# Kernel tuning notes

Hardware: AMD Instinct MI355X
Metric: run time of the kernel (lower is better)

## Reference

```python
import jax, jax.numpy as jnp
import numpy as np

N_NODES = 100000
N_EDGES = 1200000
IN_DIM, HID, OUT = 128, 64, 64


def setup_inputs() -> dict:
    key = jax.random.key(0)
    ks = jax.random.split(key, 16)
    s = 0.05
    return {
        "x": jax.random.normal(ks[0], (N_NODES, IN_DIM), jnp.float32),
        "fc_w": jax.random.normal(ks[1], (IN_DIM, HID), jnp.float32) * s,
        "fc_b": jnp.zeros((HID,), jnp.float32),
        "conv1_w": jax.random.normal(ks[2], (IN_DIM, HID), jnp.float32) * s,
        "conv1_b": jnp.zeros((HID,), jnp.float32),
        "fc1_w": jax.random.normal(ks[3], (2 * HID, OUT), jnp.float32) * s,
        "fc1_b": jnp.zeros((OUT,), jnp.float32),
        "conv2_w": jax.random.normal(ks[4], (2 * HID, OUT), jnp.float32) * s,
        "conv2_b": jnp.zeros((OUT,), jnp.float32),
        "fc2_w": jax.random.normal(ks[5], (OUT, 1), jnp.float32) * s,
        "fc2_b": jnp.zeros((1,), jnp.float32),
        "conv3_w": jax.random.normal(ks[6], (OUT, 1), jnp.float32) * s,
        "conv3_b": jnp.zeros((1,), jnp.float32),
        "edge_index": jax.random.randint(ks[7], (2, N_EDGES), 0, N_NODES, jnp.int64 if jax.config.jax_enable_x64 else jnp.int32),
    }


def gcn_conv(h_in, w, b, row, col, norm, n_nodes):
    # PyG GCNConv (no self loops): scatter_add(norm * (XW)[row]) at col, + bias
    h = h_in @ w                                  # [N, F_out]
    msg = h[row] * norm[:, None]                  # [E, F_out]
    out = jax.ops.segment_sum(msg, col, num_segments=n_nodes)
    return out + b


def reference(x, fc_w, fc_b, conv1_w, conv1_b, fc1_w, fc1_b, conv2_w, conv2_b,
              fc2_w, fc2_b, conv3_w, conv3_b, edge_index):
    n = x.shape[0]
    row, col = edge_index[0], edge_index[1]
    # symmetric normalization: deg over destination nodes (unit edge weights)
    deg = jax.ops.segment_sum(jnp.ones(row.shape[0], x.dtype), col, num_segments=n)
    dinv = jnp.where(deg > 0, jax.lax.rsqrt(jnp.maximum(deg, 1.0)), 0.0)
    norm = dinv[row] * dinv[col]                  # [E]

    x1 = jax.nn.relu(x @ fc_w + fc_b)             # MLP branch [N, HID]
    x2 = jax.nn.relu(gcn_conv(x, conv1_w, conv1_b, row, col, norm, n))
    x3 = jnp.concatenate([x1, x2], axis=1)        # [N, 2*HID]
    x5 = jax.nn.relu(x3 @ fc1_w + fc1_b)
    x6 = jax.nn.relu(gcn_conv(x3, conv2_w, conv2_b, row, col, norm, n))
    x7 = x5 + x6                                  # residual combine [N, OUT]
    x9 = x7 @ fc2_w + fc2_b
    x10 = gcn_conv(x7, conv3_w, conv3_b, row, col, norm, n)
    return x9 + x10                               # [N, 1]
```

## Files before the change

### kernel.cpp

```cpp
#include <hip/hip_runtime.h>

#define IN_DIM 128
#define HID 64
#define RB_SHIFT 10
#define RB 1024
#define NBMAX 128
#define MAXBIN 16384
#define PCH 2048

typedef short bf16x8 __attribute__((ext_vector_type(8)));
typedef float f32x4  __attribute__((ext_vector_type(4)));

__device__ __forceinline__ float relu(float v) { return v > 0.f ? v : 0.f; }

__device__ __forceinline__ unsigned short f2bf(float f) {
    unsigned u = __float_as_uint(f);
    u += 0x7FFFu + ((u >> 16) & 1u);
    return (unsigned short)(u >> 16);
}
__device__ __forceinline__ float bflo(unsigned u) { return __uint_as_float(u << 16); }
__device__ __forceinline__ float bfhi(unsigned u) { return __uint_as_float(u & 0xFFFF0000u); }

__global__ __launch_bounds__(256) void k_wprep(const float* __restrict__ W1a,
                                               const float* __restrict__ W2a,
                                               const float* __restrict__ W1b,
                                               const float* __restrict__ W2b,
                                               unsigned short* __restrict__ Wt,
                                               int* __restrict__ binCursor, int NR) {
    if (blockIdx.x == 0 && threadIdx.x < NR) binCursor[threadIdx.x] = threadIdx.x * MAXBIN;
    const int t = blockIdx.x * 256 + threadIdx.x;
    if (t >= 2 * 4 * 8 * 64) return;
    const int lane = t & 63;
    const int c = (t >> 6) & 7;
    const int kc = (t >> 9) & 3;
    const int layer = t >> 11;
    const int col = c * 16 + (lane & 15);
    const int k0 = kc * 32 + (lane >> 4) * 8;
    const float* W1 = layer ? W1b : W1a;
    const float* W2 = layer ? W2b : W2a;
    const float* src = (col < 64) ? (W1 + col) : (W2 + (col - 64));
    unsigned short v[8];
#pragma unroll
    for (int j = 0; j < 8; j++) v[j] = f2bf(src[(size_t)(k0 + j) * 64]);
    *(ushort4*)(Wt + (size_t)t * 8) = make_ushort4(v[0], v[1], v[2], v[3]);
    *(ushort4*)(Wt + (size_t)t * 8 + 4) = make_ushort4(v[4], v[5], v[6], v[7]);
}

__global__ __launch_bounds__(256) void k_part(const int* __restrict__ row,
                                              const int* __restrict__ col,
                                              int* __restrict__ binCursor,
                                              int2* __restrict__ part, int E) {
    __shared__ int lcur[NBMAX], gbase[NBMAX];
    const int tid = threadIdx.x;
    const int e0 = blockIdx.x * PCH;
    const int cnt = min(PCH, E - e0);
    if (tid < NBMAX) lcur[tid] = 0;
    __syncthreads();
    int rr[8], cc[8], pp[8];
    if (cnt == PCH) {
#pragma unroll
        for (int h = 0; h < 2; h++) {
            const int4 c4 = *(const int4*)(col + e0 + h * 1024 + tid * 4);
            const int4 r4 = *(const int4*)(row + e0 + h * 1024 + tid * 4);
            cc[h * 4 + 0] = c4.x; cc[h * 4 + 1] = c4.y;
            cc[h * 4 + 2] = c4.z; cc[h * 4 + 3] = c4.w;
            rr[h * 4 + 0] = r4.x; rr[h * 4 + 1] = r4.y;
            rr[h * 4 + 2] = r4.z; rr[h * 4 + 3] = r4.w;
        }
    } else {
#pragma unroll
        for (int j = 0; j < 8; j++) {
            const int e = e0 + j * 256 + tid;
            if (e < e0 + cnt) { rr[j] = row[e]; cc[j] = col[e]; }
            else cc[j] = -1;
        }
    }
#pragma unroll
    for (int j = 0; j < 8; j++)
        if (cc[j] >= 0) pp[j] = atomicAdd(&lcur[cc[j] >> RB_SHIFT], 1);
    __syncthreads();
    if (tid < NBMAX && lcur[tid] > 0)
        gbase[tid] = atomicAdd(&binCursor[tid], lcur[tid]);
    __syncthreads();
#pragma unroll
    for (int j = 0; j < 8; j++)
        if (cc[j] >= 0)
            part[gbase[cc[j] >> RB_SHIFT] + pp[j]] = make_int2(rr[j], cc[j]);
}

__global__ __launch_bounds__(256) void k_csrA(const int* __restrict__ binCursor,
                                              const int2* __restrict__ part,
                                              int* __restrict__ degi,
                                              float* __restrict__ dinv,
                                              int* __restrict__ start, int N) {
    __shared__ int cnt[RB];
    __shared__ int psum[256];
    const int b = blockIdx.x;
    const int lo = b << RB_SHIFT;
    const int tid = threadIdx.x;
    for (int i = tid; i < RB; i += 256) cnt[i] = 0;
    __syncthreads();
    const int base = b * MAXBIN;
    const int tot = binCursor[b] - base;
    for (int i = tid; i < tot; i += 256)
        atomicAdd(&cnt[part[base + i].y - lo], 1);
    __syncthreads();
    const int i0 = tid * 4;
    const int c0 = cnt[i0], c1 = cnt[i0 + 1], c2 = cnt[i0 + 2], c3 = cnt[i0 + 3];
    const int s = c0 + c1 + c2 + c3;
    psum[tid] = s;
    __syncthreads();
    for (int off = 1; off < 256; off <<= 1) {
        int t = (tid >= off) ? psum[tid - off] : 0;
        __syncthreads();
        psum[tid] += t;
        __syncthreads();
    }
    const int e = psum[tid] - s;
    const int offs[4] = {e, e + c0, e + c0 + c1, e + c0 + c1 + c2};
    const int cs[4] = {c0, c1, c2, c3};
#pragma unroll
    for (int j = 0; j < 4; j++) {
        const int n = lo + i0 + j;
        if (n < N) {
            degi[n] = cs[j];
            start[n] = base + offs[j];
            dinv[n] = cs[j] > 0 ? rsqrtf((float)cs[j]) : 0.f;
        }
    }
}

__global__ __launch_bounds__(256) void k_csrB(const int* __restrict__ binCursor,
                                              const int2* __restrict__ part,
                                              const int* __restrict__ start,
                                              const float* __restrict__ dinv,
                                              int2* __restrict__ rw, int N) {
    __shared__ int curs[RB];
    __shared__ float dv[RB];
    const int b = blockIdx.x;
    const int lo = b << RB_SHIFT;
    const int tid = threadIdx.x;
    for (int i = tid; i < RB; i += 256) {
        const int n = lo + i;
        curs[i] = (n < N) ? start[n] : 0;
        dv[i] = (n < N) ? dinv[n] : 0.f;
    }
    __syncthreads();
    const int base = b * MAXBIN;
    const int tot = binCursor[b] - base;
    for (int i = tid; i < tot; i += 256) {
        const int2 v = part[base + i];
        const int li = v.y - lo;
        const int pos = atomicAdd(&curs[li], 1);
        rw[pos] = make_int2(v.x, __float_as_int(dinv[v.x] * dv[li]));
    }
}

template <int LAYER>
__global__ __launch_bounds__(256) void k_gemm(const float* __restrict__ XF,
                                              const unsigned short* __restrict__ X1B,
                                              const unsigned short* __restrict__ X2B,
                                              const unsigned short* __restrict__ Wt,
                                              const float* __restrict__ B1,
                                              float* __restrict__ O1f,
                                              unsigned short* __restrict__ O1b,
                                              unsigned short* __restrict__ O2,
                                              int N) {
    const int tid = threadIdx.x;
    const int wave = tid >> 6;
    const int lane = tid & 63;
    const int quad = lane >> 4;
    const int lm = lane & 15;
    const int n0 = blockIdx.x * 64 + wave * 16;
    if (n0 >= N) return;
    const int nrow = min(n0 + lm, N - 1);

    f32x4 acc[8];
#pragma unroll
    for (int c = 0; c < 8; c++) acc[c] = (f32x4){0.f, 0.f, 0.f, 0.f};

#pragma unroll
    for (int kc = 0; kc < 4; kc++) {
        const int k0 = kc * 32 + quad * 8;
        bf16x8 a;
        if (LAYER == 1) {
            const float* s = XF + (size_t)nrow * IN_DIM + k0;
            const float4 q0 = *(const float4*)s;
            const float4 q1 = *(const float4*)(s + 4);
            a[0] = (short)f2bf(q0.x); a[1] = (short)f2bf(q0.y);
            a[2] = (short)f2bf(q0.z); a[3] = (short)f2bf(q0.w);
            a[4] = (short)f2bf(q1.x); a[5] = (short)f2bf(q1.y);
            a[6] = (short)f2bf(q1.z); a[7] = (short)f2bf(q1.w);
        } else {
            const unsigned short* s = (kc < 2) ? (X1B + (size_t)nrow * 64 + k0)
                                               : (X2B + (size_t)nrow * 64 + (k0 - 64));
            a = *(const bf16x8*)s;
        }
#pragma unroll
        for (int c = 0; c < 8; c++) {
            const bf16x8 b = *(const bf16x8*)(Wt + (size_t)((kc * 8 + c) * 64 + lane) * 8);
            acc[c] = __builtin_amdgcn_mfma_f32_16x16x32_bf16(a, b, acc[c], 0, 0, 0);
        }
    }

    const int nb = n0 + quad * 4;
#pragma unroll
    for (int c = 0; c < 4; c++) {
        const int col = c * 16 + lm;
        const float b = B1[col];
#pragma unroll
        for (int r = 0; r < 4; r++) {
            const int n = nb + r;
            if (n < N) {
                const float v = relu(acc[c][r] + b);
                if (LAYER == 1) O1b[(size_t)n * 64 + col] = f2bf(v);
                else            O1f[(size_t)n * 64 + col] = v;
            }
        }
    }
#pragma unroll
    for (int c = 4; c < 8; c++) {
        const int col = (c - 4) * 16 + lm;
#pragma unroll
        for (int r = 0; r < 4; r++) {
            const int n = nb + r;
            if (n < N) O2[(size_t)n * 64 + col] = f2bf(acc[c][r]);
        }
    }
}

template <int MODE>
__global__ __launch_bounds__(256) void k_gather(const int* __restrict__ start,
                                                const int* __restrict__ degi,
                                                const int2* __restrict__ rw,
                                                const unsigned short* __restrict__ H,
                                                const float* __restrict__ CB,
                                                unsigned short* __restrict__ OXB,
                                                const float* __restrict__ X5,
                                                const float* __restrict__ FC2W,
                                                const float* __restrict__ FC2B,
                                                const float* __restrict__ C3W,
                                                const float* __restrict__ C3B,
                                                float* __restrict__ H3,
                                                float* __restrict__ OUT, int N) {
    const int l = threadIdx.x & 15;
    const int d = blockIdx.x * 16 + (threadIdx.x >> 4);
    if (d >= N) return;
    int s = start[d];
    const int e2 = s + degi[d];
    float a0 = 0.f, a1 = 0.f, a2 = 0.f, a3 = 0.f;
    for (; s + 3 < e2; s += 4) {
        const int2 ea = rw[s], eb = rw[s + 1], ec = rw[s + 2], ed = rw[s + 3];
        const uint2 ua = *(const uint2*)(H + (size_t)ea.x * 64 + l * 4);
        const uint2 ub = *(const uint2*)(H + (size_t)eb.x * 64 + l * 4);
        const uint2 uc = *(const uint2*)(H + (size_t)ec.x * 64 + l * 4);
        const uint2 ud = *(const uint2*)(H + (size_t)ed.x * 64 + l * 4);
        const float wa = __int_as_float(ea.y), wb = __int_as_float(eb.y);
        const float wc = __int_as_float(ec.y), wd = __int_as_float(ed.y);
        a0 += wa * bflo(ua.x); a1 += wa * bfhi(ua.x);
        a2 += wa * bflo(ua.y); a3 += wa * bfhi(ua.y);
        a0 += wb * bflo(ub.x); a1 += wb * bfhi(ub.x);
        a2 += wb * bflo(ub.y); a3 += wb * bfhi(ub.y);
        a0 += wc * bflo(uc.x); a1 += wc * bfhi(uc.x);
        a2 += wc * bflo(uc.y); a3 += wc * bfhi(uc.y);
        a0 += wd * bflo(ud.x); a1 += wd * bfhi(ud.x);
        a2 += wd * bflo(ud.y); a3 += wd * bfhi(ud.y);
    }
    for (; s < e2; ++s) {
        const int2 ea = rw[s];
        const uint2 ua = *(const uint2*)(H + (size_t)ea.x * 64 + l * 4);
        const float wa = __int_as_float(ea.y);
        a0 += wa * bflo(ua.x); a1 += wa * bfhi(ua.x);
        a2 += wa * bflo(ua.y); a3 += wa * bfhi(ua.y);
    }
    const float4 cb = *(const float4*)(CB + l * 4);
    if (MODE == 1) {
        ushort4 o;
        o.x = f2bf(relu(a0 + cb.x)); o.y = f2bf(relu(a1 + cb.y));
        o.z = f2bf(relu(a2 + cb.z)); o.w = f2bf(relu(a3 + cb.w));
        *(ushort4*)(OXB + (size_t)d * 64 + l * 4) = o;
    } else {
        const float4 x5v = *(const float4*)(X5 + (size_t)d * 64 + l * 4);
        const float v0 = x5v.x + relu(a0 + cb.x);
        const float v1 = x5v.y + relu(a1 + cb.y);
        const float v2 = x5v.z + relu(a2 + cb.z);
        const float v3 = x5v.w + relu(a3 + cb.w);
        const float4 w9 = *(const float4*)(FC2W + l * 4);
        const float4 wX = *(const float4*)(C3W + l * 4);
        float p9 = v0 * w9.x + v1 * w9.y + v2 * w9.z + v3 * w9.w;
        float p10 = v0 * wX.x + v1 * wX.y + v2 * wX.z + v3 * wX.w;
#pragma unroll
        for (int m = 1; m < 16; m <<= 1) {
            p9 += __shfl_xor(p9, m, 64);
            p10 += __shfl_xor(p10, m, 64);
        }
        if (l == 0) {
            OUT[d] = p9 + FC2B[0] + C3B[0];
            H3[d] = p10;
        }
    }
}

__global__ __launch_bounds__(256) void k_gather1f(const int* __restrict__ start,
                                                  const int* __restrict__ degi,
                                                  const int2* __restrict__ rw,
                                                  const float* __restrict__ H3,
                                                  float* __restrict__ OUT, int N) {
    const int d = blockIdx.x * 256 + threadIdx.x;
    if (d >= N) return;
    int s = start[d];
    const int e2 = s + degi[d];
    float acc = 0.f;
    for (; s + 3 < e2; s += 4) {
        const int2 a = rw[s], b = rw[s + 1], c = rw[s + 2], e = rw[s + 3];
        acc += H3[a.x] * __int_as_float(a.y);
        acc += H3[b.x] * __int_as_float(b.y);
        acc += H3[c.x] * __int_as_float(c.y);
        acc += H3[e.x] * __int_as_float(e.y);
    }
    for (; s < e2; ++s) {
        const int2 a = rw[s];
        acc += H3[a.x] * __int_as_float(a.y);
    }
    OUT[d] += acc;
}

extern "C" void kernel_launch(void* const* d_in, const int* in_sizes, int n_in,
                              void* d_out, int out_size, void* d_ws, size_t ws_size,
                              hipStream_t stream) {
    const float* x    = (const float*)d_in[0];
    const float* fcw  = (const float*)d_in[1];
    const float* fcb  = (const float*)d_in[2];
    const float* c1w  = (const float*)d_in[3];
    const float* c1b  = (const float*)d_in[4];
    const float* f1w  = (const float*)d_in[5];
    const float* f1b  = (const float*)d_in[6];
    const float* c2w  = (const float*)d_in[7];
    const float* c2b  = (const float*)d_in[8];
    const float* f2w  = (const float*)d_in[9];
    const float* f2b  = (const float*)d_in[10];
    const float* c3w  = (const float*)d_in[11];
    const float* c3b  = (const float*)d_in[12];
    const int*   ei   = (const int*)d_in[13];

    const int N = in_sizes[0] / IN_DIM;
    const int E = in_sizes[13] / 2;
    const int* row = ei;
    const int* col = ei + E;
    float* out = (float*)d_out;

    const int NR = (N + RB - 1) >> RB_SHIFT;

    const size_t Npad = ((size_t)N + 127) & ~(size_t)127;
    const size_t NF = (size_t)N * 64;
    const size_t REG = (size_t)NR * MAXBIN;
    int*   binCur = (int*)d_ws;
    int*   degi   = binCur + NBMAX;
    float* dinv   = (float*)(degi + Npad);
    int*   start  = (int*)(dinv + Npad);
    unsigned short* Wt = (unsigned short*)(start + Npad);
    int2*  part   = (int2*)(Wt + 2 * 16384);
    int2*  rw     = part + REG;
    unsigned short* x1bf = (unsigned short*)(rw + REG);
    unsigned short* h1   = x1bf + NF;
    unsigned short* x2bf = h1 + NF;
    float* x5     = (float*)(x2bf + NF);
    float* h3     = x5 + NF;
    unsigned short* h2 = h1;

    const int gN = (N + 255) / 256;
    const int gG = (N + 63) / 64;
    const int gW = (N + 15) / 16;
    const int gP = (E + PCH - 1) / PCH;

    k_wprep<<<16, 256, 0, stream>>>(fcw, c1w, f1w, c2w, Wt, binCur, NR);
    k_part<<<gP, 256, 0, stream>>>(row, col, binCur, part, E);
    k_csrA<<<NR, 256, 0, stream>>>(binCur, part, degi, dinv, start, N);
    k_csrB<<<NR, 256, 0, stream>>>(binCur, part, start, dinv, rw, N);

    k_gemm<1><<<gG, 256, 0, stream>>>(x, nullptr, nullptr, Wt, fcb,
                                      nullptr, x1bf, h1, N);
    k_gather<1><<<gW, 256, 0, stream>>>(start, degi, rw, h1, c1b, x2bf,
                                        nullptr, nullptr, nullptr, nullptr,
                                        nullptr, nullptr, nullptr, N);

    k_gemm<2><<<gG, 256, 0, stream>>>(nullptr, x1bf, x2bf, Wt + 16384, f1b,
                                      x5, nullptr, h2, N);
    k_gather<2><<<gW, 256, 0, stream>>>(start, degi, rw, h2, c2b, nullptr,
                                        x5, f2w, f2b, c3w, c3b, h3, out, N);
    k_gather1f<<<gN, 256, 0, stream>>>(start, degi, rw, h3, out, N);
}
```

Before: 285.5 us.

## Factor GCN edge norm into per-node dinv scaling and merge CSR kernels

```diff
diff --git a/kernel.cpp b/kernel.cpp
--- a/kernel.cpp
+++ b/kernel.cpp
@@ -88,11 +88,12 @@
             part[gbase[cc[j] >> RB_SHIFT] + pp[j]] = make_int2(rr[j], cc[j]);
 }
 
-__global__ __launch_bounds__(256) void k_csrA(const int* __restrict__ binCursor,
-                                              const int2* __restrict__ part,
-                                              int* __restrict__ degi,
-                                              float* __restrict__ dinv,
-                                              int* __restrict__ start, int N) {
+__global__ __launch_bounds__(256) void k_csr(const int* __restrict__ binCursor,
+                                             const int2* __restrict__ part,
+                                             int* __restrict__ degi,
+                                             float* __restrict__ dinv,
+                                             int* __restrict__ start,
+                                             int* __restrict__ rs, int N) {
     __shared__ int cnt[RB];
     __shared__ int psum[256];
     const int b = blockIdx.x;
@@ -127,32 +128,13 @@
             start[n] = base + offs[j];
             dinv[n] = cs[j] > 0 ? rsqrtf((float)cs[j]) : 0.f;
         }
-    }
-}
-
-__global__ __launch_bounds__(256) void k_csrB(const int* __restrict__ binCursor,
-                                              const int2* __restrict__ part,
-                                              const int* __restrict__ start,
-                                              const float* __restrict__ dinv,
-                                              int2* __restrict__ rw, int N) {
-    __shared__ int curs[RB];
-    __shared__ float dv[RB];
-    const int b = blockIdx.x;
-    const int lo = b << RB_SHIFT;
-    const int tid = threadIdx.x;
-    for (int i = tid; i < RB; i += 256) {
-        const int n = lo + i;
-        curs[i] = (n < N) ? start[n] : 0;
-        dv[i] = (n < N) ? dinv[n] : 0.f;
-    }
-    __syncthreads();
-    const int base = b * MAXBIN;
-    const int tot = binCursor[b] - base;
+        cnt[i0 + j] = base + offs[j];
+    }
+    __syncthreads();
     for (int i = tid; i < tot; i += 256) {
         const int2 v = part[base + i];
-        const int li = v.y - lo;
-        const int pos = atomicAdd(&curs[li], 1);
-        rw[pos] = make_int2(v.x, __float_as_int(dinv[v.x] * dv[li]));
+        const int pos = atomicAdd(&cnt[v.y - lo], 1);
+        rs[pos] = v.x;
     }
 }
 
@@ -162,6 +144,7 @@
                                               const unsigned short* __restrict__ X2B,
                                               const unsigned short* __restrict__ Wt,
                                               const float* __restrict__ B1,
+                                              const float* __restrict__ dinv,
                                               float* __restrict__ O1f,
                                               unsigned short* __restrict__ O1b,
                                               unsigned short* __restrict__ O2,
@@ -204,6 +187,9 @@
     }
 
     const int nb = n0 + quad * 4;
+    float dvv[4];
+#pragma unroll
+    for (int r = 0; r < 4; r++) dvv[r] = (nb + r < N) ? dinv[nb + r] : 0.f;
 #pragma unroll
     for (int c = 0; c < 4; c++) {
         const int col = c * 16 + lm;
@@ -224,7 +210,7 @@
 #pragma unroll
         for (int r = 0; r < 4; r++) {
             const int n = nb + r;
-            if (n < N) O2[(size_t)n * 64 + col] = f2bf(acc[c][r]);
+            if (n < N) O2[(size_t)n * 64 + col] = f2bf(acc[c][r] * dvv[r]);
         }
     }
 }
@@ -232,8 +218,9 @@
 template <int MODE>
 __global__ __launch_bounds__(256) void k_gather(const int* __restrict__ start,
                                                 const int* __restrict__ degi,
-                                                const int2* __restrict__ rw,
+                                                const int* __restrict__ rs,
                                                 const unsigned short* __restrict__ H,
+                                                const float* __restrict__ dinv,
                                                 const float* __restrict__ CB,
                                                 unsigned short* __restrict__ OXB,
                                                 const float* __restrict__ X5,
@@ -243,68 +230,73 @@
                                                 const float* __restrict__ C3B,
                                                 float* __restrict__ H3,
                                                 float* __restrict__ OUT, int N) {
-    const int l = threadIdx.x & 15;
-    const int d = blockIdx.x * 16 + (threadIdx.x >> 4);
+    const int l = threadIdx.x & 7;
+    const int d = blockIdx.x * 32 + (threadIdx.x >> 3);
     if (d >= N) return;
     int s = start[d];
     const int e2 = s + degi[d];
     float a0 = 0.f, a1 = 0.f, a2 = 0.f, a3 = 0.f;
+    float a4 = 0.f, a5 = 0.f, a6 = 0.f, a7 = 0.f;
+#define ACC8(u)                                                          \
+    a0 += bflo(u.x); a1 += bfhi(u.x); a2 += bflo(u.y); a3 += bfhi(u.y);  \
+    a4 += bflo(u.z); a5 += bfhi(u.z); a6 += bflo(u.w); a7 += bfhi(u.w);
     for (; s + 3 < e2; s += 4) {
-        const int2 ea = rw[s], eb = rw[s + 1], ec = rw[s + 2], ed = rw[s + 3];
-        const uint2 ua = *(const uint2*)(H + (size_t)ea.x * 64 + l * 4);
-        const uint2 ub = *(const uint2*)(H + (size_t)eb.x * 64 + l * 4);
-        const uint2 uc = *(const uint2*)(H + (size_t)ec.x * 64 + l * 4);
-        const uint2 ud = *(const uint2*)(H + (size_t)ed.x * 64 + l * 4);
-        const float wa = __int_as_float(ea.y), wb = __int_as_float(eb.y);
-        const float wc = __int_as_float(ec.y), wd = __int_as_float(ed.y);
-        a0 += wa * bflo(ua.x); a1 += wa * bfhi(ua.x);
-        a2 += wa * bflo(ua.y); a3 += wa * bfhi(ua.y);
-        a0 += wb * bflo(ub.x); a1 += wb * bfhi(ub.x);
-        a2 += wb * bflo(ub.y); a3 += wb * bfhi(ub.y);
-        a0 += wc * bflo(uc.x); a1 += wc * bfhi(uc.x);
-        a2 += wc * bflo(uc.y); a3 += wc * bfhi(uc.y);
-        a0 += wd * bflo(ud.x); a1 += wd * bfhi(ud.x);
-        a2 += wd * bflo(ud.y); a3 += wd * bfhi(ud.y);
+        const int4 e4 = *(const int4*)(rs + s);
+        const uint4 ua = *(const uint4*)(H + (size_t)e4.x * 64 + l * 8);
+        const uint4 ub = *(const uint4*)(H + (size_t)e4.y * 64 + l * 8);
+        const uint4 uc = *(const uint4*)(H + (size_t)e4.z * 64 + l * 8);
+        const uint4 ud = *(const uint4*)(H + (size_t)e4.w * 64 + l * 8);
+        ACC8(ua) ACC8(ub) ACC8(uc) ACC8(ud)
     }
     for (; s < e2; ++s) {
-        const int2 ea = rw[s];
-        const uint2 ua = *(const uint2*)(H + (size_t)ea.x * 64 + l * 4);
-        const float wa = __int_as_float(ea.y);
-        a0 += wa * bflo(ua.x); a1 += wa * bfhi(ua.x);
-        a2 += wa * bflo(ua.y); a3 += wa * bfhi(ua.y);
-    }
-    const float4 cb = *(const float4*)(CB + l * 4);
+        const uint4 ua = *(const uint4*)(H + (size_t)rs[s] * 64 + l * 8);
+        ACC8(ua)
+    }
+#undef ACC8
+    const float dd = dinv[d];
+    const float4 cba = *(const float4*)(CB + l * 8);
+    const float4 cbb = *(const float4*)(CB + l * 8 + 4);
+    const float r0 = relu(dd * a0 + cba.x), r1 = relu(dd * a1 + cba.y);
+    const float r2 = relu(dd * a2 + cba.z), r3 = relu(dd * a3 + cba.w);
+    const float r4 = relu(dd * a4 + cbb.x), r5 = relu(dd * a5 + cbb.y);
+    const float r6 = relu(dd * a6 + cbb.z), r7 = relu(dd * a7 + cbb.w);
     if (MODE == 1) {
-        ushort4 o;
-        o.x = f2bf(relu(a0 + cb.x)); o.y = f2bf(relu(a1 + cb.y));
-        o.z = f2bf(relu(a2 + cb.z)); o.w = f2bf(relu(a3 + cb.w));
-        *(ushort4*)(OXB + (size_t)d * 64 + l * 4) = o;
+        uint4 o;
+        o.x = (unsigned)f2bf(r0) | ((unsigned)f2bf(r1) << 16);
+        o.y = (unsigned)f2bf(r2) | ((unsigned)f2bf(r3) << 16);
+        o.z = (unsigned)f2bf(r4) | ((unsigned)f2bf(r5) << 16);
+        o.w = (unsigned)f2bf(r6) | ((unsigned)f2bf(r7) << 16);
+        *(uint4*)(OXB + (size_t)d * 64 + l * 8) = o;
     } else {
-        const float4 x5v = *(const float4*)(X5 + (size_t)d * 64 + l * 4);
-        const float v0 = x5v.x + relu(a0 + cb.x);
-        const float v1 = x5v.y + relu(a1 + cb.y);
-        const float v2 = x5v.z + relu(a2 + cb.z);
-        const float v3 = x5v.w + relu(a3 + cb.w);
-        const float4 w9 = *(const float4*)(FC2W + l * 4);
-        const float4 wX = *(const float4*)(C3W + l * 4);
-        float p9 = v0 * w9.x + v1 * w9.y + v2 * w9.z + v3 * w9.w;
-        float p10 = v0 * wX.x + v1 * wX.y + v2 * wX.z + v3 * wX.w;
-#pragma unroll
-        for (int m = 1; m < 16; m <<= 1) {
+        const float4 xa = *(const float4*)(X5 + (size_t)d * 64 + l * 8);
+        const float4 xb = *(const float4*)(X5 + (size_t)d * 64 + l * 8 + 4);
+        const float v0 = xa.x + r0, v1 = xa.y + r1, v2 = xa.z + r2, v3 = xa.w + r3;
+        const float v4 = xb.x + r4, v5 = xb.y + r5, v6 = xb.z + r6, v7 = xb.w + r7;
+        const float4 w9a = *(const float4*)(FC2W + l * 8);
+        const float4 w9b = *(const float4*)(FC2W + l * 8 + 4);
+        const float4 wXa = *(const float4*)(C3W + l * 8);
+        const float4 wXb = *(const float4*)(C3W + l * 8 + 4);
+        float p9 = v0 * w9a.x + v1 * w9a.y + v2 * w9a.z + v3 * w9a.w
+                 + v4 * w9b.x + v5 * w9b.y + v6 * w9b.z + v7 * w9b.w;
+        float p10 = v0 * wXa.x + v1 * wXa.y + v2 * wXa.z + v3 * wXa.w
+                  + v4 * wXb.x + v5 * wXb.y + v6 * wXb.z + v7 * wXb.w;
+#pragma unroll
+        for (int m = 1; m < 8; m <<= 1) {
             p9 += __shfl_xor(p9, m, 64);
             p10 += __shfl_xor(p10, m, 64);
         }
         if (l == 0) {
             OUT[d] = p9 + FC2B[0] + C3B[0];
-            H3[d] = p10;
+            H3[d] = p10 * dd;
         }
     }
 }
 
 __global__ __launch_bounds__(256) void k_gather1f(const int* __restrict__ start,
                                                   const int* __restrict__ degi,
-                                                  const int2* __restrict__ rw,
+                                                  const int* __restrict__ rs,
                                                   const float* __restrict__ H3,
+                                                  const float* __restrict__ dinv,
                                                   float* __restrict__ OUT, int N) {
     const int d = blockIdx.x * 256 + threadIdx.x;
     if (d >= N) return;
@@ -312,17 +304,11 @@
     const int e2 = s + degi[d];
     float acc = 0.f;
     for (; s + 3 < e2; s += 4) {
-        const int2 a = rw[s], b = rw[s + 1], c = rw[s + 2], e = rw[s + 3];
-        acc += H3[a.x] * __int_as_float(a.y);
-        acc += H3[b.x] * __int_as_float(b.y);
-        acc += H3[c.x] * __int_as_float(c.y);
-        acc += H3[e.x] * __int_as_float(e.y);
-    }
-    for (; s < e2; ++s) {
-        const int2 a = rw[s];
-        acc += H3[a.x] * __int_as_float(a.y);
-    }
-    OUT[d] += acc;
+        const int4 e4 = *(const int4*)(rs + s);
+        acc += H3[e4.x] + H3[e4.y] + H3[e4.z] + H3[e4.w];
+    }
+    for (; s < e2; ++s) acc += H3[rs[s]];
+    OUT[d] += acc * dinv[d];
 }
 
 extern "C" void kernel_launch(void* const* d_in, const int* in_sizes, int n_in,
@@ -360,8 +346,8 @@
     int*   start  = (int*)(dinv + Npad);
     unsigned short* Wt = (unsigned short*)(start + Npad);
     int2*  part   = (int2*)(Wt + 2 * 16384);
-    int2*  rw     = part + REG;
-    unsigned short* x1bf = (unsigned short*)(rw + REG);
+    int*   rs     = (int*)(part + REG);
+    unsigned short* x1bf = (unsigned short*)(rs + REG);
     unsigned short* h1   = x1bf + NF;
     unsigned short* x2bf = h1 + NF;
     float* x5     = (float*)(x2bf + NF);
@@ -370,23 +356,22 @@
 
     const int gN = (N + 255) / 256;
     const int gG = (N + 63) / 64;
-    const int gW = (N + 15) / 16;
+    const int gW = (N + 31) / 32;
     const int gP = (E + PCH - 1) / PCH;
 
     k_wprep<<<16, 256, 0, stream>>>(fcw, c1w, f1w, c2w, Wt, binCur, NR);
     k_part<<<gP, 256, 0, stream>>>(row, col, binCur, part, E);
-    k_csrA<<<NR, 256, 0, stream>>>(binCur, part, degi, dinv, start, N);
-    k_csrB<<<NR, 256, 0, stream>>>(binCur, part, start, dinv, rw, N);
-
-    k_gemm<1><<<gG, 256, 0, stream>>>(x, nullptr, nullptr, Wt, fcb,
+    k_csr<<<NR, 256, 0, stream>>>(binCur, part, degi, dinv, start, rs, N);
+
+    k_gemm<1><<<gG, 256, 0, stream>>>(x, nullptr, nullptr, Wt, fcb, dinv,
                                       nullptr, x1bf, h1, N);
-    k_gather<1><<<gW, 256, 0, stream>>>(start, degi, rw, h1, c1b, x2bf,
+    k_gather<1><<<gW, 256, 0, stream>>>(start, degi, rs, h1, dinv, c1b, x2bf,
                                         nullptr, nullptr, nullptr, nullptr,
                                         nullptr, nullptr, nullptr, N);
 
-    k_gemm<2><<<gG, 256, 0, stream>>>(nullptr, x1bf, x2bf, Wt + 16384, f1b,
+    k_gemm<2><<<gG, 256, 0, stream>>>(nullptr, x1bf, x2bf, Wt + 16384, f1b, dinv,
                                       x5, nullptr, h2, N);
-    k_gather<2><<<gW, 256, 0, stream>>>(start, degi, rw, h2, c2b, nullptr,
+    k_gather<2><<<gW, 256, 0, stream>>>(start, degi, rs, h2, dinv, c2b, nullptr,
                                         x5, f2w, f2b, c3w, c3b, h3, out, N);
-    k_gather1f<<<gN, 256, 0, stream>>>(start, degi, rw, h3, out, N);
-}
+    k_gather1f<<<gN, 256, 0, stream>>>(start, degi, rs, h3, dinv, out, N);
+}
```

Result: faster. 260.2 us (-8.9%).
